# Performance work log

Measured on AMD Instinct MI355X. Metric: run time of the kernel, lower is better.

Reference implementation:

```python
import jax, jax.numpy as jnp
import numpy as np

B, C, H, W = 8, 512, 48, 48
TC = 512  # text channels


def conv1x1(x, w, b):
    # x: [B,Cin,H,W], w: [Cout,Cin], b: [Cout] -> [B,Cout,H,W]
    return jnp.einsum('bchw,oc->bohw', x, w) + b[None, :, None, None]


def setup_inputs() -> dict:
    key = jax.random.key(0)
    ks = jax.random.split(key, 8)
    s = 1.0 / np.sqrt(C)
    return {
        'img_feat': jax.random.normal(ks[0], (B, C, H, W), jnp.float32),
        'text_feat': jax.random.normal(ks[1], (B, TC, H, W), jnp.float32),
        'w_tp': jax.random.normal(ks[2], (C, TC), jnp.float32) * s,
        'b_tp': jnp.zeros((C,), jnp.float32),
        'w_q': jax.random.normal(ks[3], (C, C), jnp.float32) * s,
        'b_q': jnp.zeros((C,), jnp.float32),
        'w_k': jax.random.normal(ks[4], (C, C), jnp.float32) * s,
        'b_k': jnp.zeros((C,), jnp.float32),
        'w_v': jax.random.normal(ks[5], (C, C), jnp.float32) * s,
        'b_v': jnp.zeros((C,), jnp.float32),
        'scale': jnp.array([0.1], jnp.float32),
    }


def reference(img_feat, text_feat, w_tp, b_tp, w_q, b_q, w_k, b_k, w_v, b_v, scale):
    tf = conv1x1(text_feat, w_tp, b_tp)          # [B,C,H,W]
    Q = conv1x1(img_feat, w_q, b_q)
    K = conv1x1(tf, w_k, b_k)
    V = conv1x1(tf, w_v, b_v)
    # full spatial cross-attention: scores [B,H,W,Hk,Wk]
    attn = jnp.einsum('bchw,bcHW->bhwHW', Q, K) * scale[0]
    b_, h_, w_, hk, wk = attn.shape
    attn = jax.nn.softmax(attn.reshape(b_, h_, w_, hk * wk), axis=-1)
    attn = attn.reshape(b_, h_, w_, hk, wk)
    out = jnp.einsum('bhwHW,bcHW->bchw', attn, V)
    return img_feat + out
```

## Files before the change

kernel.cpp:

```cpp
#include <hip/hip_runtime.h>
#include <stdint.h>

#define NB   8
#define CCH  512
#define NPIX 2304

typedef __attribute__((ext_vector_type(8))) short s16x8;
typedef __attribute__((ext_vector_type(4))) float fx4;

__device__ __forceinline__ unsigned short f2bf(float x) {
  union { float f; unsigned u; } v; v.f = x;
  return (unsigned short)((v.u + 0x7FFFu + ((v.u >> 16) & 1u)) >> 16);
}
__device__ __forceinline__ float bf2f(unsigned short b) {
  union { unsigned u; float f; } v; v.u = ((unsigned)b) << 16;
  return v.f;
}

__device__ __forceinline__ void gload16(const unsigned short* g, unsigned short* l) {
  auto gp = reinterpret_cast<const __attribute__((address_space(1))) unsigned int*>(
      reinterpret_cast<uintptr_t>(g));
  auto lp = reinterpret_cast<__attribute__((address_space(3))) unsigned int*>(
      reinterpret_cast<uintptr_t>(l));
  __builtin_amdgcn_global_load_lds(gp, lp, 16, 0, 0);
}

__global__ __launch_bounds__(256)
void k_transpose_cast(const float* __restrict__ in, unsigned short* __restrict__ outp,
                      int R, int Cc) {
  __shared__ float tile[32][33];
  const int b = blockIdx.z;
  const int c0 = blockIdx.x * 32;
  const int r0 = blockIdx.y * 32;
  const float* src = in + (size_t)b * R * Cc;
  unsigned short* dst = outp + (size_t)b * R * Cc;
  const int tc = threadIdx.x & 31, tr = threadIdx.x >> 5;
  #pragma unroll
  for (int i = 0; i < 32; i += 8)
    tile[tr + i][tc] = src[(size_t)(r0 + tr + i) * Cc + (c0 + tc)];
  __syncthreads();
  #pragma unroll
  for (int i = 0; i < 32; i += 8)
    dst[(size_t)(c0 + tr + i) * R + (r0 + tc)] = f2bf(tile[tc][tr + i]);
}

__global__ __launch_bounds__(256)
void k_cast_bf16(const float* __restrict__ in, unsigned short* __restrict__ outp, int n) {
  const int i = (blockIdx.x * 256 + threadIdx.x) * 4;
  if (i < n) {
    const float4 v = *(const float4*)(in + i);
    ushort4 o;
    o.x = f2bf(v.x); o.y = f2bf(v.y); o.z = f2bf(v.z); o.w = f2bf(v.w);
    *(ushort4*)(outp + i) = o;
  }
}

__global__ __launch_bounds__(256)
void k_bias_fold(const float* __restrict__ wk, const float* __restrict__ bk,
                 const float* __restrict__ wv, const float* __restrict__ bv,
                 const float* __restrict__ btp, float* __restrict__ bkf,
                 float* __restrict__ bvf) {
  const int o = blockIdx.x * 256 + threadIdx.x;
  if (o < CCH) {
    float sk = bk[o], sv = bv[o];
    for (int t = 0; t < CCH; ++t) {
      const float bt = btp[t];
      sk += wk[(size_t)o * CCH + t] * bt;
      sv += wv[(size_t)o * CCH + t] * bt;
    }
    bkf[o] = sk; bvf[o] = sv;
  }
}

template<int BM, int BN, int MODE>
__global__ __launch_bounds__(256)
void k_gemm_nt(const unsigned short* __restrict__ A, const unsigned short* __restrict__ B,
               const float* __restrict__ bias, const float* __restrict__ scale_p,
               unsigned short* __restrict__ Cb, float* __restrict__ Cf,
               const float* __restrict__ resid, float* __restrict__ lsum,
               int nkb, int tilesN, long astride, long bstride, long cstride, int ldc)
{
  constexpr int WM = BM / 2, WN = BN / 2, MI = WM / 16, NI = WN / 16;
  constexpr int ABB = 2 * (BM + BN) * 32 * 2;
  constexpr int EPB = WM * (BN + 8) * 2;
  constexpr int SMB = (ABB > EPB) ? ABB : EPB;
  __shared__ __align__(16) char smem[SMB];
  auto As  = reinterpret_cast<unsigned short (*)[BM][32]>(smem);
  auto Bs  = reinterpret_cast<unsigned short (*)[BN][32]>(smem + (size_t)2 * BM * 32 * 2);
  auto epi = reinterpret_cast<unsigned short (*)[BN + 8]>(smem);

  const int gx = gridDim.x;
  const int nwg = gx * gridDim.y;
  const int id = blockIdx.y * gx + blockIdx.x;
  const int swz = (id & 7) * (nwg >> 3) + (id >> 3);
  const int bb = swz / gx;
  const int tile = swz % gx;

  const unsigned short* Ap = A + (size_t)bb * astride;
  const unsigned short* Bp = B + (size_t)bb * bstride;
  const int tm = tile / tilesN, tn = tile % tilesN;
  const int row0 = tm * BM, col0 = tn * BN;
  const int t = threadIdx.x, wave = t >> 6, lane = t & 63;
  const int lo = lane & 15, hi = lane >> 4;
  const int wr = (wave >> 1) * WM, wc = (wave & 1) * WN;
  const int ldk = nkb * 32;
  const int l4r = lane >> 2, l4c = (lane & 3) * 8;

  fx4 acc[MI][NI];
  #pragma unroll
  for (int mi = 0; mi < MI; ++mi)
    #pragma unroll
    for (int ni = 0; ni < NI; ++ni)
      #pragma unroll
      for (int r = 0; r < 4; ++r) acc[mi][ni][r] = 0.f;

  auto stage = [&](int buf, int kb) {
    #pragma unroll
    for (int j = 0; j < BM / 64; ++j) {
      const int rb = wave * (BM / 64) * 16 + j * 16;
      gload16(Ap + (size_t)(row0 + rb + l4r) * ldk + kb * 32 + l4c, &As[buf][rb][0]);
    }
    #pragma unroll
    for (int j = 0; j < BN / 64; ++j) {
      const int rb = wave * (BN / 64) * 16 + j * 16;
      gload16(Bp + (size_t)(col0 + rb + l4r) * ldk + kb * 32 + l4c, &Bs[buf][rb][0]);
    }
  };

  stage(0, 0);
  __syncthreads();

  for (int kb = 0; kb < nkb; ++kb) {
    const int cur = kb & 1;
    if (kb + 1 < nkb) stage(cur ^ 1, kb + 1);
    s16x8 af[MI], bf[NI];
    #pragma unroll
    for (int mi = 0; mi < MI; ++mi) af[mi] = *(const s16x8*)&As[cur][wr + mi * 16 + lo][hi * 8];
    #pragma unroll
    for (int ni = 0; ni < NI; ++ni) bf[ni] = *(const s16x8*)&Bs[cur][wc + ni * 16 + lo][hi * 8];
    #pragma unroll
    for (int mi = 0; mi < MI; ++mi)
      #pragma unroll
      for (int ni = 0; ni < NI; ++ni)
        acc[mi][ni] = __builtin_amdgcn_mfma_f32_16x16x32_bf16(af[mi], bf[ni], acc[mi][ni], 0, 0, 0);
    if (kb + 1 < nkb) __syncthreads();
  }

  if (MODE == 6) {
    #pragma unroll
    for (int ni = 0; ni < NI; ++ni) {
      const int col = col0 + wc + ni * 16 + lo;
      const float li = 1.0f / lsum[(size_t)bb * NPIX + col];
      #pragma unroll
      for (int mi = 0; mi < MI; ++mi) {
        #pragma unroll
        for (int r = 0; r < 4; ++r) {
          const int row = row0 + wr + mi * 16 + hi * 4 + r;
          const size_t idx = (size_t)bb * cstride + (size_t)row * ldc + col;
          Cf[idx] = resid[idx] + acc[mi][ni][r] * li;
        }
      }
    }
  } else {
    const float smul = (MODE == 1 && scale_p) ? scale_p[0] : 1.f;
    __syncthreads();
    #pragma unroll
    for (int h = 0; h < 2; ++h) {
      if ((wave >> 1) == h) {
        #pragma unroll
        for (int ni = 0; ni < NI; ++ni) {
          const int colg = col0 + wc + ni * 16 + lo;
          const float cb = (MODE == 1) ? bias[colg] : 0.f;
          #pragma unroll
          for (int mi = 0; mi < MI; ++mi) {
            #pragma unroll
            for (int r = 0; r < 4; ++r) {
              float v = acc[mi][ni][r];
              if (MODE == 1) v = (v + cb) * smul;
              if (MODE == 2) v = v + bias[row0 + h * WM + mi * 16 + hi * 4 + r];
              if (MODE == 5) v = __expf(v);
              epi[mi * 16 + hi * 4 + r][wc + ni * 16 + lo] = f2bf(v);
            }
          }
        }
      }
      __syncthreads();
      constexpr int CPR = BN / 8;
      constexpr int ITER = (WM * BN) / (256 * 8);
      #pragma unroll
      for (int i = 0; i < ITER; ++i) {
        const int c = t + i * 256;
        const int rl = c / CPR;
        const int cb8 = c % CPR;
        const s16x8 val = *(const s16x8*)&epi[rl][cb8 * 8];
        const int rowg = row0 + h * WM + rl;
        *(s16x8*)(Cb + (size_t)bb * cstride + (size_t)rowg * ldc + col0 + cb8 * 8) = val;
        if (MODE == 5) {
          float ps = 0.f;
          #pragma unroll
          for (int j = 0; j < 8; ++j) ps += bf2f((unsigned short)val[j]);
          #pragma unroll
          for (int m = 1; m < CPR; m <<= 1) ps += __shfl_xor(ps, m);
          if ((lane & (CPR - 1)) == 0) atomicAdd(&lsum[(size_t)bb * NPIX + rowg], ps);
        }
      }
      __syncthreads();
    }
  }
}

extern "C" void kernel_launch(void* const* d_in, const int* in_sizes, int n_in,
                              void* d_out, int out_size, void* d_ws, size_t ws_size,
                              hipStream_t stream) {
  const float* img   = (const float*)d_in[0];
  const float* text  = (const float*)d_in[1];
  const float* w_tp  = (const float*)d_in[2];
  const float* b_tp  = (const float*)d_in[3];
  const float* w_q   = (const float*)d_in[4];
  const float* b_q   = (const float*)d_in[5];
  const float* w_k   = (const float*)d_in[6];
  const float* b_k   = (const float*)d_in[7];
  const float* w_v   = (const float*)d_in[8];
  const float* b_v   = (const float*)d_in[9];
  const float* scale = (const float*)d_in[10];
  float* outp = (float*)d_out;

  char* ws = (char*)d_ws;
  const size_t SZ_BT = (size_t)NB * NPIX * CCH * sizeof(unsigned short);
  const size_t SZ_W  = (size_t)CCH * CCH * sizeof(unsigned short);
  const size_t SZ_S  = (size_t)4 * NPIX * NPIX * sizeof(unsigned short);

  unsigned short* Qtb  = (unsigned short*)ws;  ws += SZ_BT;
  unsigned short* Ktb  = (unsigned short*)ws;  ws += SZ_BT;
  unsigned short* Vcb  = (unsigned short*)ws;  ws += SZ_BT;
  unsigned short* wtpT = (unsigned short*)ws;  ws += SZ_W;
  unsigned short* wqb  = (unsigned short*)ws;  ws += SZ_W;
  unsigned short* wkb  = (unsigned short*)ws;  ws += SZ_W;
  unsigned short* wvb  = (unsigned short*)ws;  ws += SZ_W;
  unsigned short* WKf  = (unsigned short*)ws;  ws += SZ_W;
  unsigned short* WVf  = (unsigned short*)ws;  ws += SZ_W;
  float* bkf  = (float*)ws;                    ws += 2048;
  float* bvf  = (float*)ws;                    ws += 2048;
  float* lsum = (float*)ws;                    ws += (size_t)4 * NPIX * sizeof(float);
  unsigned short* Sb   = (unsigned short*)ws;  ws += SZ_S;
  unsigned short* IMGt  = Sb;
  unsigned short* TEXTt = Sb + (size_t)NB * NPIX * CCH;

  dim3 blk(256);
  const int nW = CCH * CCH;

  k_transpose_cast<<<dim3(NPIX / 32, CCH / 32, NB), blk, 0, stream>>>(img,  IMGt,  CCH, NPIX);
  k_transpose_cast<<<dim3(NPIX / 32, CCH / 32, NB), blk, 0, stream>>>(text, TEXTt, CCH, NPIX);
  k_transpose_cast<<<dim3(CCH / 32, CCH / 32, 1),   blk, 0, stream>>>(w_tp, wtpT,  CCH, CCH);
  k_cast_bf16<<<dim3(nW / 1024), blk, 0, stream>>>(w_q, wqb, nW);
  k_cast_bf16<<<dim3(nW / 1024), blk, 0, stream>>>(w_k, wkb, nW);
  k_cast_bf16<<<dim3(nW / 1024), blk, 0, stream>>>(w_v, wvb, nW);
  k_bias_fold<<<dim3(2), blk, 0, stream>>>(w_k, b_k, w_v, b_v, b_tp, bkf, bvf);
  k_gemm_nt<128,128,0><<<dim3(16, 1), blk, 0, stream>>>(
      wkb, wtpT, nullptr, nullptr, WKf, nullptr, nullptr, nullptr, 16, 4, 0, 0, 0, CCH);
  k_gemm_nt<128,128,0><<<dim3(16, 1), blk, 0, stream>>>(
      wvb, wtpT, nullptr, nullptr, WVf, nullptr, nullptr, nullptr, 16, 4, 0, 0, 0, CCH);
  k_gemm_nt<128,128,1><<<dim3(576, 1), blk, 0, stream>>>(
      IMGt, wqb, b_q, scale, Qtb, nullptr, nullptr, nullptr, 16, 4, 0, 0, 0, CCH);
  k_gemm_nt<128,128,1><<<dim3(576, 1), blk, 0, stream>>>(
      TEXTt, WKf, bkf, nullptr, Ktb, nullptr, nullptr, nullptr, 16, 4, 0, 0, 0, CCH);
  k_gemm_nt<64,128,2><<<dim3(144, NB), blk, 0, stream>>>(
      WVf, TEXTt, bvf, nullptr, Vcb, nullptr, nullptr, nullptr,
      16, 18, 0, (long)NPIX * CCH, (long)CCH * NPIX, NPIX);

  for (int chunk = 0; chunk < 2; ++chunk) {
    const long bo = (long)chunk * 4;
    hipMemsetAsync(lsum, 0, (size_t)4 * NPIX * sizeof(float), stream);
    k_gemm_nt<128,256,5><<<dim3(162, 4), blk, 0, stream>>>(
        Qtb + bo * NPIX * CCH, Ktb + bo * NPIX * CCH, nullptr, nullptr,
        Sb, nullptr, nullptr, lsum,
        16, 9, (long)NPIX * CCH, (long)NPIX * CCH, (long)NPIX * NPIX, NPIX);
    k_gemm_nt<64,128,6><<<dim3(144, 4), blk, 0, stream>>>(
        Vcb + bo * CCH * NPIX, Sb, nullptr, nullptr,
        nullptr, outp + bo * CCH * NPIX, img + bo * CCH * NPIX, lsum,
        72, 18, (long)CCH * NPIX, (long)NPIX * NPIX, (long)CCH * NPIX, NPIX);
  }
}
```

Baseline: 480.4 us.

## Merge preprocessing launches and shrink score GEMM tile to 128x128

Combines the img and text transpose-casts into one launch over a doubled z grid, and merges the three weight casts into one launch indexed by blockIdx.y. This cuts kernel launch overhead in the preprocessing phase. Separately, the QK^T score GEMM tile drops from 128x256 to 128x128, doubling the grid to 324x4 blocks. That gives more parallelism and occupancy, at the cost of less data reuse per block and more lsum atomics.

```diff
diff --git a/kernel.cpp b/kernel.cpp
--- a/kernel.cpp
+++ b/kernel.cpp
@@ -26,26 +26,48 @@
 }
 
 __global__ __launch_bounds__(256)
+void k_transpose_cast2(const float* __restrict__ in0, unsigned short* __restrict__ out0,
+                       const float* __restrict__ in1, unsigned short* __restrict__ out1) {
+  __shared__ float tile[32][33];
+  const int z = blockIdx.z;
+  const int b = z & (NB - 1);
+  const float* src = (z < NB ? in0 : in1) + (size_t)b * CCH * NPIX;
+  unsigned short* dst = (z < NB ? out0 : out1) + (size_t)b * CCH * NPIX;
+  const int c0 = blockIdx.x * 32;
+  const int r0 = blockIdx.y * 32;
+  const int tc = threadIdx.x & 31, tr = threadIdx.x >> 5;
+  #pragma unroll
+  for (int i = 0; i < 32; i += 8)
+    tile[tr + i][tc] = src[(size_t)(r0 + tr + i) * NPIX + (c0 + tc)];
+  __syncthreads();
+  #pragma unroll
+  for (int i = 0; i < 32; i += 8)
+    dst[(size_t)(c0 + tr + i) * CCH + (r0 + tc)] = f2bf(tile[tc][tr + i]);
+}
+
+__global__ __launch_bounds__(256)
 void k_transpose_cast(const float* __restrict__ in, unsigned short* __restrict__ outp,
                       int R, int Cc) {
   __shared__ float tile[32][33];
-  const int b = blockIdx.z;
   const int c0 = blockIdx.x * 32;
   const int r0 = blockIdx.y * 32;
-  const float* src = in + (size_t)b * R * Cc;
-  unsigned short* dst = outp + (size_t)b * R * Cc;
   const int tc = threadIdx.x & 31, tr = threadIdx.x >> 5;
   #pragma unroll
   for (int i = 0; i < 32; i += 8)
-    tile[tr + i][tc] = src[(size_t)(r0 + tr + i) * Cc + (c0 + tc)];
+    tile[tr + i][tc] = in[(size_t)(r0 + tr + i) * Cc + (c0 + tc)];
   __syncthreads();
   #pragma unroll
   for (int i = 0; i < 32; i += 8)
-    dst[(size_t)(c0 + tr + i) * R + (r0 + tc)] = f2bf(tile[tc][tr + i]);
-}
-
-__global__ __launch_bounds__(256)
-void k_cast_bf16(const float* __restrict__ in, unsigned short* __restrict__ outp, int n) {
+    outp[(size_t)(c0 + tr + i) * R + (r0 + tc)] = f2bf(tile[tc][tr + i]);
+}
+
+__global__ __launch_bounds__(256)
+void k_cast_bf16_3(const float* __restrict__ s0, unsigned short* __restrict__ d0,
+                   const float* __restrict__ s1, unsigned short* __restrict__ d1,
+                   const float* __restrict__ s2, unsigned short* __restrict__ d2, int n) {
+  const int which = blockIdx.y;
+  const float* in = which == 0 ? s0 : which == 1 ? s1 : s2;
+  unsigned short* outp = which == 0 ? d0 : which == 1 ? d1 : d2;
   const int i = (blockIdx.x * 256 + threadIdx.x) * 4;
   if (i < n) {
     const float4 v = *(const float4*)(in + i);
@@ -249,12 +271,9 @@
   dim3 blk(256);
   const int nW = CCH * CCH;
 
-  k_transpose_cast<<<dim3(NPIX / 32, CCH / 32, NB), blk, 0, stream>>>(img,  IMGt,  CCH, NPIX);
-  k_transpose_cast<<<dim3(NPIX / 32, CCH / 32, NB), blk, 0, stream>>>(text, TEXTt, CCH, NPIX);
-  k_transpose_cast<<<dim3(CCH / 32, CCH / 32, 1),   blk, 0, stream>>>(w_tp, wtpT,  CCH, CCH);
-  k_cast_bf16<<<dim3(nW / 1024), blk, 0, stream>>>(w_q, wqb, nW);
-  k_cast_bf16<<<dim3(nW / 1024), blk, 0, stream>>>(w_k, wkb, nW);
-  k_cast_bf16<<<dim3(nW / 1024), blk, 0, stream>>>(w_v, wvb, nW);
+  k_transpose_cast2<<<dim3(NPIX / 32, CCH / 32, 2 * NB), blk, 0, stream>>>(img, IMGt, text, TEXTt);
+  k_transpose_cast<<<dim3(CCH / 32, CCH / 32, 1), blk, 0, stream>>>(w_tp, wtpT, CCH, CCH);
+  k_cast_bf16_3<<<dim3(nW / 1024, 3), blk, 0, stream>>>(w_q, wqb, w_k, wkb, w_v, wvb, nW);
   k_bias_fold<<<dim3(2), blk, 0, stream>>>(w_k, b_k, w_v, b_v, b_tp, bkf, bvf);
   k_gemm_nt<128,128,0><<<dim3(16, 1), blk, 0, stream>>>(
       wkb, wtpT, nullptr, nullptr, WKf, nullptr, nullptr, nullptr, 16, 4, 0, 0, 0, CCH);
@@ -271,10 +290,10 @@
   for (int chunk = 0; chunk < 2; ++chunk) {
     const long bo = (long)chunk * 4;
     hipMemsetAsync(lsum, 0, (size_t)4 * NPIX * sizeof(float), stream);
-    k_gemm_nt<128,256,5><<<dim3(162, 4), blk, 0, stream>>>(
+    k_gemm_nt<128,128,5><<<dim3(324, 4), blk, 0, stream>>>(
         Qtb + bo * NPIX * CCH, Ktb + bo * NPIX * CCH, nullptr, nullptr,
         Sb, nullptr, nullptr, lsum,
-        16, 9, (long)NPIX * CCH, (long)NPIX * CCH, (long)NPIX * NPIX, NPIX);
+        16, 18, (long)NPIX * CCH, (long)NPIX * CCH, (long)NPIX * NPIX, NPIX);
     k_gemm_nt<64,128,6><<<dim3(144, 4), blk, 0, stream>>>(
         Vcb + bo * CCH * NPIX, Sb, nullptr, nullptr,
         nullptr, outp + bo * CCH * NPIX, img + bo * CCH * NPIX, lsum,
```

After: 421.6 us. -12.2%, faster.
